# Kernel optimization log

Measured on AMD Instinct MI355X. Metric: run time of the kernel, lower is better.

The kernel has to match this reference:

```python
import jax, jax.numpy as jnp
import numpy as np

N, K, D = 8192, 512, 4096

def setup_inputs() -> dict:
    key = jax.random.key(0)
    k1, k2, k3 = jax.random.split(key, 3)
    features = jax.random.normal(k1, (N, K), dtype=jnp.float32)
    w = jax.random.normal(k2, (D, N), dtype=jnp.float32)
    E = jax.random.normal(k3, (K, D), dtype=jnp.float32) / np.sqrt(K)  # embed_matrix (k x d)
    b = jnp.zeros((D,), dtype=jnp.float32)  # bias initialized to zeros in the module
    return {"features": features, "w": w, "E": E, "b": b}

def reference(features, w, E, b):
    # Linear: y = features @ E + b  -> (N, D)   (torch weight is E.mT, so x @ W.T == x @ E)
    y = features @ E + b
    # diag(y @ w): equivalent to row-wise dot products, same math without the NxN matmul
    return jnp.einsum("nd,dn->n", y, w)
```

## Files before the change

kernel.cpp:

```cpp
#include <hip/hip_runtime.h>

#define N_DIM 8192
#define K_DIM 512
#define D_DIM 4096

typedef __bf16 bf16x8 __attribute__((ext_vector_type(8)));
typedef float  f32x16 __attribute__((ext_vector_type(16)));
typedef unsigned short u16x8 __attribute__((ext_vector_type(8)));

__device__ __forceinline__ unsigned short f2bf(float f) {
    union { float f; unsigned int u; } v; v.f = f;
    unsigned int r = v.u + 0x7FFF + ((v.u >> 16) & 1);
    return (unsigned short)(r >> 16);
}

__global__ __launch_bounds__(256) void transpose_E(const float* __restrict__ E,
                                                   unsigned short* __restrict__ ET) {
    __shared__ float tile[64][65];
    const int d0 = blockIdx.x * 64;
    const int k0 = blockIdx.y * 64;
    const int tid = threadIdx.x;
    const int r  = tid / 16;
    const int c4 = (tid % 16) * 4;
#pragma unroll
    for (int p = 0; p < 4; ++p) {
        int k = p * 16 + r;
        float4 v = *reinterpret_cast<const float4*>(E + (size_t)(k0 + k) * D_DIM + d0 + c4);
        tile[k][c4 + 0] = v.x; tile[k][c4 + 1] = v.y;
        tile[k][c4 + 2] = v.z; tile[k][c4 + 3] = v.w;
    }
    __syncthreads();
#pragma unroll
    for (int p = 0; p < 4; ++p) {
        int d = p * 16 + r;
        ushort4 o;
        o.x = f2bf(tile[c4 + 0][d]);
        o.y = f2bf(tile[c4 + 1][d]);
        o.z = f2bf(tile[c4 + 2][d]);
        o.w = f2bf(tile[c4 + 3][d]);
        *reinterpret_cast<ushort4*>(ET + (size_t)(d0 + d) * K_DIM + k0 + c4) = o;
    }
}

__global__ __launch_bounds__(256) void convert_F(const float* __restrict__ F,
                                                 unsigned short* __restrict__ FB) {
    const int idx8 = (blockIdx.x * 256 + threadIdx.x) * 8;
    float4 a = *reinterpret_cast<const float4*>(F + idx8);
    float4 b = *reinterpret_cast<const float4*>(F + idx8 + 4);
    u16x8 o;
    o[0] = f2bf(a.x); o[1] = f2bf(a.y); o[2] = f2bf(a.z); o[3] = f2bf(a.w);
    o[4] = f2bf(b.x); o[5] = f2bf(b.y); o[6] = f2bf(b.z); o[7] = f2bf(b.w);
    *reinterpret_cast<u16x8*>(FB + idx8) = o;
}

__global__ __launch_bounds__(256) void gemm_fused(const unsigned short* __restrict__ FB,
                                                  const float* __restrict__ W,
                                                  const unsigned short* __restrict__ ET,
                                                  const float* __restrict__ B,
                                                  float* __restrict__ out) {
    __shared__ unsigned short Ash[2 * 128 * 32];
    __shared__ unsigned short Bsh[2 * 128 * 32];

    const int tid  = threadIdx.x;
    const int wave = tid >> 6;
    const int lane = tid & 63;
    const int wy   = wave >> 1;
    const int wx   = wave & 1;
    const int l31  = lane & 31;
    const int half = lane >> 5;

    const int f   = blockIdx.x + ((int)gridDim.x) * blockIdx.y;
    const int xcd = f & 7;
    const int s   = f >> 3;
    const int ntile = (xcd & 3) * 16 + (s & 15);
    const int dtile = (xcd >> 2) * 16 + (s >> 4);
    const int n0 = ntile * 128;
    const int d0 = dtile * 128;

    f32x16 acc[2][2] = {};

    const int srow   = lane >> 2;
    const int schunk = (((lane & 3) ^ ((srow >> 1) & 3)) * 8);

    for (int kt = 0; kt < K_DIM / 64; ++kt) {
        const int kb = kt * 64;
#pragma unroll
        for (int p = 0; p < 2; ++p) {
#pragma unroll
            for (int jj = 0; jj < 2; ++jj) {
                const int j = wave * 2 + jj;
                const unsigned short* ga =
                    ET + (size_t)(d0 + j * 16 + srow) * K_DIM + kb + p * 32 + schunk;
                __builtin_amdgcn_global_load_lds(
                    (const __attribute__((address_space(1))) void*)ga,
                    (__attribute__((address_space(3))) void*)(Ash + p * 4096 + j * 512),
                    16, 0, 0);
                const unsigned short* gb =
                    FB + (size_t)(n0 + j * 16 + srow) * K_DIM + kb + p * 32 + schunk;
                __builtin_amdgcn_global_load_lds(
                    (const __attribute__((address_space(1))) void*)gb,
                    (__attribute__((address_space(3))) void*)(Bsh + p * 4096 + j * 512),
                    16, 0, 0);
            }
        }
        __syncthreads();

#pragma unroll
        for (int ks = 0; ks < 4; ++ks) {
            const int p = ks >> 1;
            const int c = (ks & 1) * 2 + half;
            bf16x8 af[2], bf[2];
#pragma unroll
            for (int mi = 0; mi < 2; ++mi) {
                const int R = wy * 64 + mi * 32 + l31;
                const int slot = c ^ ((R >> 1) & 3);
                af[mi] = *reinterpret_cast<const bf16x8*>(
                    Ash + p * 4096 + R * 32 + slot * 8);
            }
#pragma unroll
            for (int ni = 0; ni < 2; ++ni) {
                const int R = wx * 64 + ni * 32 + l31;
                const int slot = c ^ ((R >> 1) & 3);
                bf[ni] = *reinterpret_cast<const bf16x8*>(
                    Bsh + p * 4096 + R * 32 + slot * 8);
            }
#pragma unroll
            for (int mi = 0; mi < 2; ++mi)
#pragma unroll
                for (int ni = 0; ni < 2; ++ni)
                    acc[mi][ni] = __builtin_amdgcn_mfma_f32_32x32x16_bf16(
                        af[mi], bf[ni], acc[mi][ni], 0, 0, 0);
        }
        __syncthreads();
    }

    const int nb = n0 + wx * 64;
    float part0 = 0.f, part1 = 0.f;
#pragma unroll
    for (int mi = 0; mi < 2; ++mi) {
        const int dbase = d0 + wy * 64 + mi * 32 + 4 * half;
#pragma unroll
        for (int reg = 0; reg < 16; ++reg) {
            const int dd = dbase + (reg & 3) + 8 * (reg >> 2);
            const float bd = B[dd];
            const float* wr = W + (size_t)dd * N_DIM + nb;
            part0 += (acc[mi][0][reg] + bd) * __builtin_nontemporal_load(wr + l31);
            part1 += (acc[mi][1][reg] + bd) * __builtin_nontemporal_load(wr + 32 + l31);
        }
    }
    part0 += __shfl_xor(part0, 32);
    part1 += __shfl_xor(part1, 32);
    if (lane < 32) {
        atomicAdd(out + nb + l31, part0);
        atomicAdd(out + nb + 32 + l31, part1);
    }
}

extern "C" void kernel_launch(void* const* d_in, const int* in_sizes, int n_in,
                              void* d_out, int out_size, void* d_ws, size_t ws_size,
                              hipStream_t stream) {
    const float* F = (const float*)d_in[0];
    const float* W = (const float*)d_in[1];
    const float* E = (const float*)d_in[2];
    const float* B = (const float*)d_in[3];
    float* out = (float*)d_out;

    unsigned short* ET = (unsigned short*)d_ws;
    unsigned short* FB = (unsigned short*)((char*)d_ws + (size_t)D_DIM * K_DIM * 2);

    hipMemsetAsync(d_out, 0, (size_t)out_size * sizeof(float), stream);
    transpose_E<<<dim3(D_DIM / 64, K_DIM / 64), 256, 0, stream>>>(E, ET);
    convert_F<<<dim3(N_DIM * K_DIM / (256 * 8)), 256, 0, stream>>>(F, FB);
    gemm_fused<<<dim3(N_DIM / 128, D_DIM / 128), 256, 0, stream>>>(FB, W, ET, B, out);
}
```

Before: 237.3 us.

## Pre-swizzle E into MFMA fragment layout and load A operands directly from global

The transpose kernel now writes E as bf16 in a layout where each 32-row, 16-k block is stored exactly as a wave's MFMA A-fragment register order. The GEMM then drops the A-tile LDS staging and reads those fragments straight from global memory with one 16-byte load per lane, which halves LDS traffic and shared-memory footprint. The cost is that A loads are no longer shared through LDS, so each wave issues its own global loads and relies on cache hits, and load latency now sits in the MFMA loop without explicit prefetch.

```diff
diff --git a/kernel.cpp b/kernel.cpp
--- a/kernel.cpp
+++ b/kernel.cpp
@@ -15,30 +15,35 @@
 }
 
 __global__ __launch_bounds__(256) void transpose_E(const float* __restrict__ E,
-                                                   unsigned short* __restrict__ ET) {
+                                                   unsigned short* __restrict__ ETf) {
     __shared__ float tile[64][65];
     const int d0 = blockIdx.x * 64;
     const int k0 = blockIdx.y * 64;
     const int tid = threadIdx.x;
-    const int r  = tid / 16;
-    const int c4 = (tid % 16) * 4;
+    {
+        const int r  = tid / 16;
+        const int c4 = (tid % 16) * 4;
 #pragma unroll
-    for (int p = 0; p < 4; ++p) {
-        int k = p * 16 + r;
-        float4 v = *reinterpret_cast<const float4*>(E + (size_t)(k0 + k) * D_DIM + d0 + c4);
-        tile[k][c4 + 0] = v.x; tile[k][c4 + 1] = v.y;
-        tile[k][c4 + 2] = v.z; tile[k][c4 + 3] = v.w;
+        for (int p = 0; p < 4; ++p) {
+            int k = p * 16 + r;
+            float4 v = *reinterpret_cast<const float4*>(E + (size_t)(k0 + k) * D_DIM + d0 + c4);
+            tile[k][c4 + 0] = v.x; tile[k][c4 + 1] = v.y;
+            tile[k][c4 + 2] = v.z; tile[k][c4 + 3] = v.w;
+        }
     }
     __syncthreads();
+    const int lane = tid & 63;
+    const int w    = tid >> 6;
+    const int dl5  = lane & 31;
+    const int k8h  = lane >> 5;
 #pragma unroll
-    for (int p = 0; p < 4; ++p) {
-        int d = p * 16 + r;
-        ushort4 o;
-        o.x = f2bf(tile[c4 + 0][d]);
-        o.y = f2bf(tile[c4 + 1][d]);
-        o.z = f2bf(tile[c4 + 2][d]);
-        o.w = f2bf(tile[c4 + 3][d]);
-        *reinterpret_cast<ushort4*>(ET + (size_t)(d0 + d) * K_DIM + k0 + c4) = o;
+    for (int q = 0; q < 2; ++q) {
+        u16x8 o;
+#pragma unroll
+        for (int j = 0; j < 8; ++j)
+            o[j] = f2bf(tile[w * 16 + k8h * 8 + j][q * 32 + dl5]);
+        const int frag = ((d0 >> 5) + q) * 32 + (k0 >> 4) + w;
+        *reinterpret_cast<u16x8*>(ETf + (size_t)frag * 512 + lane * 8) = o;
     }
 }
 
@@ -55,10 +60,9 @@
 
 __global__ __launch_bounds__(256) void gemm_fused(const unsigned short* __restrict__ FB,
                                                   const float* __restrict__ W,
-                                                  const unsigned short* __restrict__ ET,
+                                                  const unsigned short* __restrict__ ETf,
                                                   const float* __restrict__ B,
                                                   float* __restrict__ out) {
-    __shared__ unsigned short Ash[2 * 128 * 32];
     __shared__ unsigned short Bsh[2 * 128 * 32];
 
     const int tid  = threadIdx.x;
@@ -79,6 +83,9 @@
 
     f32x16 acc[2][2] = {};
 
+    const unsigned short* pa0 = ETf + (size_t)((d0 >> 5) + wy * 2 + 0) * 16384 + lane * 8;
+    const unsigned short* pa1 = ETf + (size_t)((d0 >> 5) + wy * 2 + 1) * 16384 + lane * 8;
+
     const int srow   = lane >> 2;
     const int schunk = (((lane & 3) ^ ((srow >> 1) & 3)) * 8);
 
@@ -89,12 +96,6 @@
 #pragma unroll
             for (int jj = 0; jj < 2; ++jj) {
                 const int j = wave * 2 + jj;
-                const unsigned short* ga =
-                    ET + (size_t)(d0 + j * 16 + srow) * K_DIM + kb + p * 32 + schunk;
-                __builtin_amdgcn_global_load_lds(
-                    (const __attribute__((address_space(1))) void*)ga,
-                    (__attribute__((address_space(3))) void*)(Ash + p * 4096 + j * 512),
-                    16, 0, 0);
                 const unsigned short* gb =
                     FB + (size_t)(n0 + j * 16 + srow) * K_DIM + kb + p * 32 + schunk;
                 __builtin_amdgcn_global_load_lds(
@@ -110,13 +111,8 @@
             const int p = ks >> 1;
             const int c = (ks & 1) * 2 + half;
             bf16x8 af[2], bf[2];
-#pragma unroll
-            for (int mi = 0; mi < 2; ++mi) {
-                const int R = wy * 64 + mi * 32 + l31;
-                const int slot = c ^ ((R >> 1) & 3);
-                af[mi] = *reinterpret_cast<const bf16x8*>(
-                    Ash + p * 4096 + R * 32 + slot * 8);
-            }
+            af[0] = *reinterpret_cast<const bf16x8*>(pa0 + (kt * 4 + ks) * 512);
+            af[1] = *reinterpret_cast<const bf16x8*>(pa1 + (kt * 4 + ks) * 512);
 #pragma unroll
             for (int ni = 0; ni < 2; ++ni) {
                 const int R = wx * 64 + ni * 32 + l31;
@@ -129,7 +125,7 @@
 #pragma unroll
                 for (int ni = 0; ni < 2; ++ni)
                     acc[mi][ni] = __builtin_amdgcn_mfma_f32_32x32x16_bf16(
-                        af[mi], bf[ni], acc[mi][ni], 0, 0, 0);
+                        mi == 0 ? af[0] : af[1], bf[ni], acc[mi][ni], 0, 0, 0);
         }
         __syncthreads();
     }
@@ -165,11 +161,11 @@
     const float* B = (const float*)d_in[3];
     float* out = (float*)d_out;
 
-    unsigned short* ET = (unsigned short*)d_ws;
-    unsigned short* FB = (unsigned short*)((char*)d_ws + (size_t)D_DIM * K_DIM * 2);
+    unsigned short* ETf = (unsigned short*)d_ws;
+    unsigned short* FB  = (unsigned short*)((char*)d_ws + (size_t)D_DIM * K_DIM * 2);
 
-    hipMemsetAsync(d_out, 0, (size_t)out_size * sizeof(float), stream);
-    transpose_E<<<dim3(D_DIM / 64, K_DIM / 64), 256, 0, stream>>>(E, ET);
+    (void)hipMemsetAsync(d_out, 0, (size_t)out_size * sizeof(float), stream);
+    transpose_E<<<dim3(D_DIM / 64, K_DIM / 64), 256, 0, stream>>>(E, ETf);
     convert_F<<<dim3(N_DIM * K_DIM / (256 * 8)), 256, 0, stream>>>(F, FB);
-    gemm_fused<<<dim3(N_DIM / 128, D_DIM / 128), 256, 0, stream>>>(FB, W, ET, B, out);
+    gemm_fused<<<dim3(N_DIM / 128, D_DIM / 128), 256, 0, stream>>>(FB, W, ETf, B, out);
 }
```

New measurement: 244.8 us. 1.03x slower.
